# Optimization experiments

Measured on AMD Instinct MI355X. Metric: run time of the kernel, lower is better.

The kernel has to match this reference:

```python
import jax, jax.numpy as jnp
import numpy as np

N_NODES = 100000
N_EDGES = 3200000
D_IN = 128
D_HID = 128
N_CLASSES = 64
EPS = 0.0  # GINConv default


def setup_inputs() -> dict:
    key = jax.random.key(0)
    k1, k2, k3, k4, k5, k6 = jax.random.split(key, 6)
    x = jax.random.normal(k1, (N_NODES, D_IN), dtype=jnp.float32)
    edge_index = jax.random.randint(k2, (2, N_EDGES), 0, N_NODES, dtype=jnp.int64)
    s1 = 1.0 / np.sqrt(D_IN)
    W1 = jax.random.uniform(k3, (D_HID, D_IN), minval=-s1, maxval=s1, dtype=jnp.float32)
    b1 = jax.random.uniform(k4, (D_HID,), minval=-s1, maxval=s1, dtype=jnp.float32)
    s2 = 1.0 / np.sqrt(D_HID)
    W2 = jax.random.uniform(k5, (N_CLASSES, D_HID), minval=-s2, maxval=s2, dtype=jnp.float32)
    b2 = jax.random.uniform(k6, (N_CLASSES,), minval=-s2, maxval=s2, dtype=jnp.float32)
    return {"x": x, "edge_index": edge_index, "W1": W1, "b1": b1, "W2": W2, "b2": b2}


def gin_conv(h, src, dst, W, b):
    # sum_{j in N(i)} h_j  : scatter-add of source features into target nodes
    msgs = jnp.take(h, src, axis=0)                       # [E, D]
    agg = jax.ops.segment_sum(msgs, dst, num_segments=N_NODES)  # [N, D]
    z = (1.0 + EPS) * h + agg
    return z @ W.T + b


def reference(x, edge_index, W1, b1, W2, b2):
    src = edge_index[0]
    dst = edge_index[1]
    h = gin_conv(x, src, dst, W1, b1)
    h = jax.nn.relu(h)
    # dropout p=0.5 is identity in eval mode
    out = gin_conv(h, src, dst, W2, b2)
    return out
```

## Files before the change

kernel.cpp:

```cpp
#include <hip/hip_runtime.h>
#include <stdint.h>

#define NN 100000
#define NE 3200000
#define NBK 782
#define NB  512
#define CH  6250
#define CSRCAP 4800

typedef unsigned int uint;
typedef unsigned short ushort;
typedef __attribute__((ext_vector_type(8))) short bf16x8;
typedef __attribute__((ext_vector_type(4))) float f32x4;

static __device__ __forceinline__ float bflo(uint v) {
    uint u = v << 16; return __builtin_bit_cast(float, u);
}
static __device__ __forceinline__ float bfhi(uint v) {
    uint u = v & 0xffff0000u; return __builtin_bit_cast(float, u);
}
static __device__ __forceinline__ float bfraw(uint v) {
    return __builtin_bit_cast(float, v);
}
static __device__ __forceinline__ float b2f(ushort v) {
    uint u = ((uint)v) << 16; return __builtin_bit_cast(float, u);
}
static __device__ __forceinline__ ushort f2b(float f) {
    uint u = __builtin_bit_cast(uint, f);
    u += 0x7fffu + ((u >> 16) & 1u);
    return (ushort)(u >> 16);
}
static __device__ __forceinline__ int wscan(int v, int lane) {
#pragma unroll
    for (int off = 1; off < 64; off <<= 1) {
        int t = __shfl_up(v, off);
        if (lane >= off) v += t;
    }
    return v;
}


__global__ __launch_bounds__(512) void hist2_k(const int* __restrict__ ei,
                                               int* __restrict__ hist) {
    __shared__ int hl[NBK];
    int tid = threadIdx.x, b = blockIdx.x;
    for (int k = tid; k < NBK; k += 512) hl[k] = 0;
    __syncthreads();
    int base = b * CH;
    for (int i = base + tid; i < base + CH; i += 512)
        atomicAdd(&hl[ei[NE + i] >> 7], 1);
    __syncthreads();
    for (int k = tid; k < NBK; k += 512) hist[b * NBK + k] = hl[k];
}

__global__ __launch_bounds__(64) void pbase_k(const int* __restrict__ hist,
                                              int* __restrict__ pbase,
                                              int* __restrict__ totals) {
    int k = blockIdx.x, lane = threadIdx.x;
    int carry = 0;
#pragma unroll
    for (int c = 0; c < NB / 64; ++c) {
        int b = c * 64 + lane;
        int v = hist[b * NBK + k];
        int incl = wscan(v, lane);
        pbase[b * NBK + k] = carry + incl - v;
        carry += __shfl(incl, 63);
    }
    if (lane == 0) totals[k] = carry;
}

__global__ __launch_bounds__(1024) void bscan_k(const int* __restrict__ totals,
                                                int* __restrict__ gbase,
                                                int* __restrict__ nodeptr,
                                                ushort* __restrict__ y1,
                                                ushort* __restrict__ y2) {
    __shared__ int sd[1024];
    int t = threadIdx.x;
    int v = (t < NBK) ? totals[t] : 0;
    sd[t] = v;
    __syncthreads();
    for (int off = 1; off < 1024; off <<= 1) {
        int u = (t >= off) ? sd[t - off] : 0;
        __syncthreads();
        sd[t] += u;
        __syncthreads();
    }
    int excl = sd[t] - v;
    if (t < NBK) gbase[t] = excl;
    if (t == 0) { gbase[NBK] = NE; nodeptr[NN] = NE; }
    if (t < 64) ((uint*)(y1 + (size_t)NN * 128))[t] = 0;
    if (t < 32) ((uint*)(y2 + (size_t)NN * 64))[t] = 0;
}

__global__ __launch_bounds__(512) void bfill2_k(const int* __restrict__ ei,
                                                const int* __restrict__ pbase,
                                                const int* __restrict__ gbase,
                                                uint* __restrict__ barr) {
    __shared__ int cur[NBK];
    int tid = threadIdx.x, b = blockIdx.x;
    for (int k = tid; k < NBK; k += 512)
        cur[k] = gbase[k] + pbase[b * NBK + k];
    __syncthreads();
    int base = b * CH;
    for (int i = base + tid; i < base + CH; i += 512) {
        int s = ei[i], d = ei[NE + i];
        int pos = atomicAdd(&cur[d >> 7], 1);
        barr[pos] = ((uint)(d & 127) << 17) | (uint)s;
    }
}

__global__ __launch_bounds__(256) void csr_k(const uint* __restrict__ barr,
                                             const int* __restrict__ gbase,
                                             int* __restrict__ nodeptr,
                                             uint* __restrict__ col) {
    __shared__ uint stg[CSRCAP];
    __shared__ int cnt[128], cur[128];
    int tid = threadIdx.x;
    int blk = blockIdx.x;
    int s0 = gbase[blk], s1 = gbase[blk + 1];
    int n = s1 - s0;
    bool fits = (n <= CSRCAP);
    if (tid < 128) cnt[tid] = 0;
    __syncthreads();
    if (fits) {
        for (int i = tid; i < n; i += 256) {
            uint e = barr[s0 + i];
            stg[i] = e;
            atomicAdd(&cnt[e >> 17], 1);
        }
    } else {
        for (int i = s0 + tid; i < s1; i += 256)
            atomicAdd(&cnt[barr[i] >> 17], 1);
    }
    __syncthreads();
    if (tid < 64) {
        int c0 = cnt[2 * tid], c1 = cnt[2 * tid + 1];
        int s = c0 + c1;
        int incl = wscan(s, tid);
        int excl = incl - s;
        cur[2 * tid] = excl;
        cur[2 * tid + 1] = excl + c0;
        int node = blk * 128 + 2 * tid;
        if (node < NN)     nodeptr[node]     = s0 + excl;
        if (node + 1 < NN) nodeptr[node + 1] = s0 + excl + c0;
    }
    __syncthreads();
    if (fits) {
        for (int i = tid; i < n; i += 256) {
            uint e = stg[i];
            int pos = s0 + atomicAdd(&cur[e >> 17], 1);
            col[pos] = e & 0x1FFFF;
        }
    } else {
        for (int i = s0 + tid; i < s1; i += 256) {
            uint e = barr[i];
            int pos = s0 + atomicAdd(&cur[e >> 17], 1);
            col[pos] = e & 0x1FFFF;
        }
    }
}

__global__ __launch_bounds__(256) void gemm1_k(const float* __restrict__ x,
                                               const float* __restrict__ W1,
                                               ushort* __restrict__ y1) {
    __shared__ ushort wl[128 * 136];
    int tid = threadIdx.x;
    for (int i = tid; i < 128 * 128; i += 256)
        wl[(i >> 7) * 136 + (i & 127)] = f2b(W1[i]);
    __syncthreads();

    int wave = tid >> 6, lane = tid & 63;
    int lr = lane & 15, lk = (lane >> 4) * 8;
    long rowbase = (long)blockIdx.x * 128 + wave * 32;

    f32x4 acc[2][8] = {};
    for (int kc = 0; kc < 128; kc += 32) {
        bf16x8 a[2];
#pragma unroll
        for (int m = 0; m < 2; m++) {
            long row = rowbase + m * 16 + lr;
            if (row > NN - 1) row = NN - 1;
            const float* p = x + row * 128 + kc + lk;
            float f[8];
            *(float4*)(f)     = *(const float4*)(p);
            *(float4*)(f + 4) = *(const float4*)(p + 4);
            bf16x8 t;
#pragma unroll
            for (int j = 0; j < 8; j++) t[j] = (short)f2b(f[j]);
            a[m] = t;
        }
#pragma unroll
        for (int nb = 0; nb < 8; nb++) {
            bf16x8 b = *(const bf16x8*)&wl[(nb * 16 + lr) * 136 + kc + lk];
            acc[0][nb] = __builtin_amdgcn_mfma_f32_16x16x32_bf16(a[0], b, acc[0][nb], 0, 0, 0);
            acc[1][nb] = __builtin_amdgcn_mfma_f32_16x16x32_bf16(a[1], b, acc[1][nb], 0, 0, 0);
        }
    }
    int rq = (lane >> 4) * 4;
#pragma unroll
    for (int m = 0; m < 2; m++) {
#pragma unroll
        for (int r = 0; r < 4; r++) {
            long row = rowbase + m * 16 + rq + r;
            if (row < NN) {
#pragma unroll
                for (int nb = 0; nb < 8; nb++)
                    y1[row * 128 + nb * 16 + lr] = f2b(acc[m][nb][r]);
            }
        }
    }
}

__global__ __launch_bounds__(256) void gemm2_k(const ushort* __restrict__ h,
                                               const float* __restrict__ W2,
                                               ushort* __restrict__ y2) {
    __shared__ ushort wl[64 * 136];
    int tid = threadIdx.x;
    for (int i = tid; i < 64 * 128; i += 256)
        wl[(i >> 7) * 136 + (i & 127)] = f2b(W2[i]);
    __syncthreads();

    int wave = tid >> 6, lane = tid & 63;
    int lr = lane & 15, lk = (lane >> 4) * 8;
    long rowbase = (long)blockIdx.x * 128 + wave * 32;

    f32x4 acc[2][4] = {};
    for (int kc = 0; kc < 128; kc += 32) {
        bf16x8 a[2];
#pragma unroll
        for (int m = 0; m < 2; m++) {
            long row = rowbase + m * 16 + lr;
            if (row > NN - 1) row = NN - 1;
            a[m] = *(const bf16x8*)(h + row * 128 + kc + lk);
        }
#pragma unroll
        for (int nb = 0; nb < 4; nb++) {
            bf16x8 b = *(const bf16x8*)&wl[(nb * 16 + lr) * 136 + kc + lk];
            acc[0][nb] = __builtin_amdgcn_mfma_f32_16x16x32_bf16(a[0], b, acc[0][nb], 0, 0, 0);
            acc[1][nb] = __builtin_amdgcn_mfma_f32_16x16x32_bf16(a[1], b, acc[1][nb], 0, 0, 0);
        }
    }
    int rq = (lane >> 4) * 4;
#pragma unroll
    for (int m = 0; m < 2; m++) {
#pragma unroll
        for (int r = 0; r < 4; r++) {
            long row = rowbase + m * 16 + rq + r;
            if (row < NN) {
#pragma unroll
                for (int nb = 0; nb < 4; nb++)
                    y2[row * 64 + nb * 16 + lr] = f2b(acc[m][nb][r]);
            }
        }
    }
}


__global__ __launch_bounds__(256) void agg1_k(const ushort* __restrict__ y1,
                                              const int* __restrict__ nodeptr,
                                              const uint* __restrict__ col,
                                              const float* __restrict__ b1,
                                              ushort* __restrict__ h) {
    int wid = (blockIdx.x * 256 + threadIdx.x) >> 6;
    int lane = threadIdx.x & 63;
    if (wid >= NN) return;
    int s0 = nodeptr[wid], s1 = nodeptr[wid + 1];
    int q = lane >> 4, r = lane & 15;

    float aLo[4] = {}, aHi[4] = {};
    const ushort* yr = y1 + r * 8;

    for (int i = s0; i < s1; i += 64) {
        int m = s1 - i; if (m > 64) m = 64;
        int sv = (lane < m) ? (int)col[i + lane] : NN;
        int jg = (m + 15) >> 4;
        for (int g = 0; g < jg; ++g) {
            int e0 = 16 * g + q;
            int sj0 = __shfl(sv, e0);
            int sj1 = __shfl(sv, e0 + 4);
            int sj2 = __shfl(sv, e0 + 8);
            int sj3 = __shfl(sv, e0 + 12);
            uint4 u0 = *(const uint4*)(yr + (size_t)sj0 * 128);
            uint4 u1 = *(const uint4*)(yr + (size_t)sj1 * 128);
            uint4 u2 = *(const uint4*)(yr + (size_t)sj2 * 128);
            uint4 u3 = *(const uint4*)(yr + (size_t)sj3 * 128);
            aLo[0] += bflo(u0.x); aHi[0] += bfraw(u0.x);
            aLo[1] += bflo(u0.y); aHi[1] += bfraw(u0.y);
            aLo[2] += bflo(u0.z); aHi[2] += bfraw(u0.z);
            aLo[3] += bflo(u0.w); aHi[3] += bfraw(u0.w);
            aLo[0] += bflo(u1.x); aHi[0] += bfraw(u1.x);
            aLo[1] += bflo(u1.y); aHi[1] += bfraw(u1.y);
            aLo[2] += bflo(u1.z); aHi[2] += bfraw(u1.z);
            aLo[3] += bflo(u1.w); aHi[3] += bfraw(u1.w);
            aLo[0] += bflo(u2.x); aHi[0] += bfraw(u2.x);
            aLo[1] += bflo(u2.y); aHi[1] += bfraw(u2.y);
            aLo[2] += bflo(u2.z); aHi[2] += bfraw(u2.z);
            aLo[3] += bflo(u2.w); aHi[3] += bfraw(u2.w);
            aLo[0] += bflo(u3.x); aHi[0] += bfraw(u3.x);
            aLo[1] += bflo(u3.y); aHi[1] += bfraw(u3.y);
            aLo[2] += bflo(u3.z); aHi[2] += bfraw(u3.z);
            aLo[3] += bflo(u3.w); aHi[3] += bfraw(u3.w);
        }
    }
#pragma unroll
    for (int d = 0; d < 4; ++d) {
        aLo[d] += __shfl_xor(aLo[d], 16); aLo[d] += __shfl_xor(aLo[d], 32);
        aHi[d] += __shfl_xor(aHi[d], 16); aHi[d] += __shfl_xor(aHi[d], 32);
    }
    if (q == 0) {
        uint4 s = *(const uint4*)(y1 + (size_t)wid * 128 + r * 8);
        float4 bA = *(const float4*)(b1 + r * 8);
        float4 bB = *(const float4*)(b1 + r * 8 + 4);
        float v0 = fmaxf(aLo[0] + bflo(s.x) + bA.x, 0.f);
        float v1 = fmaxf(aHi[0] + bfhi(s.x) + bA.y, 0.f);
        float v2 = fmaxf(aLo[1] + bflo(s.y) + bA.z, 0.f);
        float v3 = fmaxf(aHi[1] + bfhi(s.y) + bA.w, 0.f);
        float v4 = fmaxf(aLo[2] + bflo(s.z) + bB.x, 0.f);
        float v5 = fmaxf(aHi[2] + bfhi(s.z) + bB.y, 0.f);
        float v6 = fmaxf(aLo[3] + bflo(s.w) + bB.z, 0.f);
        float v7 = fmaxf(aHi[3] + bfhi(s.w) + bB.w, 0.f);
        uint4 o;
        o.x = (uint)f2b(v0) | ((uint)f2b(v1) << 16);
        o.y = (uint)f2b(v2) | ((uint)f2b(v3) << 16);
        o.z = (uint)f2b(v4) | ((uint)f2b(v5) << 16);
        o.w = (uint)f2b(v6) | ((uint)f2b(v7) << 16);
        *(uint4*)(h + (size_t)wid * 128 + r * 8) = o;
    }
}

__global__ __launch_bounds__(256) void agg2_k(const ushort* __restrict__ y2,
                                              const int* __restrict__ nodeptr,
                                              const uint* __restrict__ col,
                                              const float* __restrict__ b2,
                                              float* __restrict__ out) {
    int wid = (blockIdx.x * 256 + threadIdx.x) >> 6;
    int lane = threadIdx.x & 63;
    if (wid >= NN) return;
    int s0 = nodeptr[wid], s1 = nodeptr[wid + 1];
    int q = lane >> 4, r = lane & 15;

    float aLo[2] = {}, aHi[2] = {};
    const ushort* yr = y2 + r * 4;

    for (int i = s0; i < s1; i += 64) {
        int m = s1 - i; if (m > 64) m = 64;
        int sv = (lane < m) ? (int)col[i + lane] : NN;
        int jg = (m + 15) >> 4;
        for (int g = 0; g < jg; ++g) {
            int e0 = 16 * g + q;
            int sj0 = __shfl(sv, e0);
            int sj1 = __shfl(sv, e0 + 4);
            int sj2 = __shfl(sv, e0 + 8);
            int sj3 = __shfl(sv, e0 + 12);
            uint2 u0 = *(const uint2*)(yr + (size_t)sj0 * 64);
            uint2 u1 = *(const uint2*)(yr + (size_t)sj1 * 64);
            uint2 u2 = *(const uint2*)(yr + (size_t)sj2 * 64);
            uint2 u3 = *(const uint2*)(yr + (size_t)sj3 * 64);
            aLo[0] += bflo(u0.x); aHi[0] += bfraw(u0.x);
            aLo[1] += bflo(u0.y); aHi[1] += bfraw(u0.y);
            aLo[0] += bflo(u1.x); aHi[0] += bfraw(u1.x);
            aLo[1] += bflo(u1.y); aHi[1] += bfraw(u1.y);
            aLo[0] += bflo(u2.x); aHi[0] += bfraw(u2.x);
            aLo[1] += bflo(u2.y); aHi[1] += bfraw(u2.y);
            aLo[0] += bflo(u3.x); aHi[0] += bfraw(u3.x);
            aLo[1] += bflo(u3.y); aHi[1] += bfraw(u3.y);
        }
    }
#pragma unroll
    for (int d = 0; d < 2; ++d) {
        aLo[d] += __shfl_xor(aLo[d], 16); aLo[d] += __shfl_xor(aLo[d], 32);
        aHi[d] += __shfl_xor(aHi[d], 16); aHi[d] += __shfl_xor(aHi[d], 32);
    }
    if (q == 0) {
        uint2 s = *(const uint2*)(y2 + (size_t)wid * 64 + r * 4);
        float4 bb = *(const float4*)(b2 + r * 4);
        float4 o;
        o.x = aLo[0] + bflo(s.x) + bb.x;
        o.y = aHi[0] + bfhi(s.x) + bb.y;
        o.z = aLo[1] + bflo(s.y) + bb.z;
        o.w = aHi[1] + bfhi(s.y) + bb.w;
        *(float4*)(out + (size_t)wid * 64 + r * 4) = o;
    }
}


static constexpr size_t alup(size_t x) { return (x + 255) & ~(size_t)255; }
static constexpr size_t OFF_HIST  = 0;
static constexpr size_t OFF_PBASE = alup(OFF_HIST  + (size_t)NB * NBK * 4);
static constexpr size_t OFF_TOT   = alup(OFF_PBASE + (size_t)NB * NBK * 4);
static constexpr size_t OFF_GBASE = alup(OFF_TOT   + NBK * 4);
static constexpr size_t OFF_NPTR  = alup(OFF_GBASE + (NBK + 1) * 4);
static constexpr size_t OFF_BARR  = alup(OFF_NPTR  + (size_t)(NN + 1) * 4);
static constexpr size_t OFF_COL   = alup(OFF_BARR  + (size_t)NE * 4);
static constexpr size_t OFF_Y1    = alup(OFF_COL   + (size_t)NE * 4);
static constexpr size_t OFF_H     = alup(OFF_Y1 + (size_t)(NN + 1) * 128 * 2);
static constexpr size_t OFF_Y2    = alup(OFF_H  + (size_t)NN * 128 * 2);

extern "C" void kernel_launch(void* const* d_in, const int* in_sizes, int n_in,
                              void* d_out, int out_size, void* d_ws, size_t ws_size,
                              hipStream_t stream) {
    const float* x  = (const float*)d_in[0];
    const int*   ei = (const int*)d_in[1];
    const float* W1 = (const float*)d_in[2];
    const float* b1 = (const float*)d_in[3];
    const float* W2 = (const float*)d_in[4];
    const float* b2 = (const float*)d_in[5];
    float* out = (float*)d_out;
    char* ws = (char*)d_ws;

    int*  hist  = (int*)(ws + OFF_HIST);
    int*  pbase = (int*)(ws + OFF_PBASE);
    int*  tot   = (int*)(ws + OFF_TOT);
    int*  gbase = (int*)(ws + OFF_GBASE);
    int*  nptr  = (int*)(ws + OFF_NPTR);
    uint* barr  = (uint*)(ws + OFF_BARR);
    uint* colA  = (uint*)(ws + OFF_COL);
    ushort* y1 = (ushort*)(ws + OFF_Y1);
    ushort* hh = (ushort*)(ws + OFF_H);
    ushort* y2 = (ushort*)(ws + OFF_Y2);

    hipLaunchKernelGGL(hist2_k,  dim3(NB),  dim3(512),  0, stream, ei, hist);
    hipLaunchKernelGGL(pbase_k,  dim3(NBK), dim3(64),   0, stream, hist, pbase, tot);
    hipLaunchKernelGGL(bscan_k,  dim3(1),   dim3(1024), 0, stream, tot, gbase, nptr, y1, y2);
    hipLaunchKernelGGL(bfill2_k, dim3(NB),  dim3(512),  0, stream, ei, pbase, gbase, barr);
    hipLaunchKernelGGL(csr_k,    dim3(NBK), dim3(256),  0, stream, barr, gbase, nptr, colA);

    hipLaunchKernelGGL(gemm1_k, dim3(782),  dim3(256), 0, stream, x, W1, y1);
    hipLaunchKernelGGL(agg1_k,  dim3(25000),dim3(256), 0, stream, y1, nptr, colA, b1, hh);
    hipLaunchKernelGGL(gemm2_k, dim3(782),  dim3(256), 0, stream, hh, W2, y2);
    hipLaunchKernelGGL(agg2_k,  dim3(25000),dim3(256), 0, stream, y2, nptr, colA, b2, out);
}
```

Before: 263.9 us.

## Split layer-1 features into two 64-wide halves to shrink gather working set

Stores the first layer's transformed features as two separate 64-column bf16 arrays, and runs the layer-1 aggregation twice, once per half. This keeps each gather pass's table (about 12.8 MB) small enough to stay resident in cache instead of a 25.6 MB table. Layer-2 aggregation is reworked so 8 lanes each load 16 bytes per row, with 8 edges per wave step. The cost is reading the CSR column indices twice and an extra kernel launch.

```diff
diff --git a/kernel.cpp b/kernel.cpp
--- a/kernel.cpp
+++ b/kernel.cpp
@@ -22,9 +22,6 @@
 static __device__ __forceinline__ float bfraw(uint v) {
     return __builtin_bit_cast(float, v);
 }
-static __device__ __forceinline__ float b2f(ushort v) {
-    uint u = ((uint)v) << 16; return __builtin_bit_cast(float, u);
-}
 static __device__ __forceinline__ ushort f2b(float f) {
     uint u = __builtin_bit_cast(uint, f);
     u += 0x7fffu + ((u >> 16) & 1u);
@@ -72,7 +69,8 @@
 __global__ __launch_bounds__(1024) void bscan_k(const int* __restrict__ totals,
                                                 int* __restrict__ gbase,
                                                 int* __restrict__ nodeptr,
-                                                ushort* __restrict__ y1,
+                                                ushort* __restrict__ y1a,
+                                                ushort* __restrict__ y1b,
                                                 ushort* __restrict__ y2) {
     __shared__ int sd[1024];
     int t = threadIdx.x;
@@ -88,8 +86,9 @@
     int excl = sd[t] - v;
     if (t < NBK) gbase[t] = excl;
     if (t == 0) { gbase[NBK] = NE; nodeptr[NN] = NE; }
-    if (t < 64) ((uint*)(y1 + (size_t)NN * 128))[t] = 0;
-    if (t < 32) ((uint*)(y2 + (size_t)NN * 64))[t] = 0;
+    if (t < 32)              ((uint*)(y1a + (size_t)NN * 64))[t] = 0;
+    else if (t < 64)         ((uint*)(y1b + (size_t)NN * 64))[t - 32] = 0;
+    else if (t < 96)         ((uint*)(y2  + (size_t)NN * 64))[t - 64] = 0;
 }
 
 __global__ __launch_bounds__(512) void bfill2_k(const int* __restrict__ ei,
@@ -162,7 +161,8 @@
 
 __global__ __launch_bounds__(256) void gemm1_k(const float* __restrict__ x,
                                                const float* __restrict__ W1,
-                                               ushort* __restrict__ y1) {
+                                               ushort* __restrict__ y1a,
+                                               ushort* __restrict__ y1b) {
     __shared__ ushort wl[128 * 136];
     int tid = threadIdx.x;
     for (int i = tid; i < 128 * 128; i += 256)
@@ -204,14 +204,18 @@
             long row = rowbase + m * 16 + rq + r;
             if (row < NN) {
 #pragma unroll
-                for (int nb = 0; nb < 8; nb++)
-                    y1[row * 128 + nb * 16 + lr] = f2b(acc[m][nb][r]);
+                for (int nb = 0; nb < 8; nb++) {
+                    ushort v = f2b(acc[m][nb][r]);
+                    if (nb < 4) y1a[row * 64 + nb * 16 + lr] = v;
+                    else        y1b[row * 64 + (nb - 4) * 16 + lr] = v;
+                }
             }
         }
     }
 }
 
-__global__ __launch_bounds__(256) void gemm2_k(const ushort* __restrict__ h,
+__global__ __launch_bounds__(256) void gemm2_k(const ushort* __restrict__ ha,
+                                               const ushort* __restrict__ hb,
                                                const float* __restrict__ W2,
                                                ushort* __restrict__ y2) {
     __shared__ ushort wl[64 * 136];
@@ -225,13 +229,16 @@
     long rowbase = (long)blockIdx.x * 128 + wave * 32;
 
     f32x4 acc[2][4] = {};
+#pragma unroll
     for (int kc = 0; kc < 128; kc += 32) {
+        const ushort* hsrc = (kc < 64) ? ha : hb;
+        int koff = kc & 63;
         bf16x8 a[2];
 #pragma unroll
         for (int m = 0; m < 2; m++) {
             long row = rowbase + m * 16 + lr;
             if (row > NN - 1) row = NN - 1;
-            a[m] = *(const bf16x8*)(h + row * 128 + kc + lk);
+            a[m] = *(const bf16x8*)(hsrc + row * 64 + koff + lk);
         }
 #pragma unroll
         for (int nb = 0; nb < 4; nb++) {
@@ -256,34 +263,34 @@
 }
 
 
-__global__ __launch_bounds__(256) void agg1_k(const ushort* __restrict__ y1,
-                                              const int* __restrict__ nodeptr,
-                                              const uint* __restrict__ col,
-                                              const float* __restrict__ b1,
-                                              ushort* __restrict__ h) {
+__global__ __launch_bounds__(256) void agg1h_k(const ushort* __restrict__ yh,
+                                               const int* __restrict__ nodeptr,
+                                               const uint* __restrict__ col,
+                                               const float* __restrict__ bh,
+                                               ushort* __restrict__ hh) {
     int wid = (blockIdx.x * 256 + threadIdx.x) >> 6;
     int lane = threadIdx.x & 63;
     if (wid >= NN) return;
     int s0 = nodeptr[wid], s1 = nodeptr[wid + 1];
-    int q = lane >> 4, r = lane & 15;
+    int o = lane >> 3, r = lane & 7;
 
     float aLo[4] = {}, aHi[4] = {};
-    const ushort* yr = y1 + r * 8;
+    const ushort* yr = yh + r * 8;
 
     for (int i = s0; i < s1; i += 64) {
         int m = s1 - i; if (m > 64) m = 64;
         int sv = (lane < m) ? (int)col[i + lane] : NN;
-        int jg = (m + 15) >> 4;
+        int jg = (m + 31) >> 5;
         for (int g = 0; g < jg; ++g) {
-            int e0 = 16 * g + q;
+            int e0 = 32 * g + o;
             int sj0 = __shfl(sv, e0);
-            int sj1 = __shfl(sv, e0 + 4);
-            int sj2 = __shfl(sv, e0 + 8);
-            int sj3 = __shfl(sv, e0 + 12);
-            uint4 u0 = *(const uint4*)(yr + (size_t)sj0 * 128);
-            uint4 u1 = *(const uint4*)(yr + (size_t)sj1 * 128);
-            uint4 u2 = *(const uint4*)(yr + (size_t)sj2 * 128);
-            uint4 u3 = *(const uint4*)(yr + (size_t)sj3 * 128);
+            int sj1 = __shfl(sv, e0 + 8);
+            int sj2 = __shfl(sv, e0 + 16);
+            int sj3 = __shfl(sv, e0 + 24);
+            uint4 u0 = *(const uint4*)(yr + (size_t)sj0 * 64);
+            uint4 u1 = *(const uint4*)(yr + (size_t)sj1 * 64);
+            uint4 u2 = *(const uint4*)(yr + (size_t)sj2 * 64);
+            uint4 u3 = *(const uint4*)(yr + (size_t)sj3 * 64);
             aLo[0] += bflo(u0.x); aHi[0] += bfraw(u0.x);
             aLo[1] += bflo(u0.y); aHi[1] += bfraw(u0.y);
             aLo[2] += bflo(u0.z); aHi[2] += bfraw(u0.z);
@@ -304,13 +311,14 @@
     }
 #pragma unroll
     for (int d = 0; d < 4; ++d) {
-        aLo[d] += __shfl_xor(aLo[d], 16); aLo[d] += __shfl_xor(aLo[d], 32);
-        aHi[d] += __shfl_xor(aHi[d], 16); aHi[d] += __shfl_xor(aHi[d], 32);
-    }
-    if (q == 0) {
-        uint4 s = *(const uint4*)(y1 + (size_t)wid * 128 + r * 8);
-        float4 bA = *(const float4*)(b1 + r * 8);
-        float4 bB = *(const float4*)(b1 + r * 8 + 4);
+        aLo[d] += __shfl_xor(aLo[d], 8);  aHi[d] += __shfl_xor(aHi[d], 8);
+        aLo[d] += __shfl_xor(aLo[d], 16); aHi[d] += __shfl_xor(aHi[d], 16);
+        aLo[d] += __shfl_xor(aLo[d], 32); aHi[d] += __shfl_xor(aHi[d], 32);
+    }
+    if (o == 0) {
+        uint4 s = *(const uint4*)(yh + (size_t)wid * 64 + r * 8);
+        float4 bA = *(const float4*)(bh + r * 8);
+        float4 bB = *(const float4*)(bh + r * 8 + 4);
         float v0 = fmaxf(aLo[0] + bflo(s.x) + bA.x, 0.f);
         float v1 = fmaxf(aHi[0] + bfhi(s.x) + bA.y, 0.f);
         float v2 = fmaxf(aLo[1] + bflo(s.y) + bA.z, 0.f);
@@ -319,12 +327,12 @@
         float v5 = fmaxf(aHi[2] + bfhi(s.z) + bB.y, 0.f);
         float v6 = fmaxf(aLo[3] + bflo(s.w) + bB.z, 0.f);
         float v7 = fmaxf(aHi[3] + bfhi(s.w) + bB.w, 0.f);
-        uint4 o;
-        o.x = (uint)f2b(v0) | ((uint)f2b(v1) << 16);
-        o.y = (uint)f2b(v2) | ((uint)f2b(v3) << 16);
-        o.z = (uint)f2b(v4) | ((uint)f2b(v5) << 16);
-        o.w = (uint)f2b(v6) | ((uint)f2b(v7) << 16);
-        *(uint4*)(h + (size_t)wid * 128 + r * 8) = o;
+        uint4 out;
+        out.x = (uint)f2b(v0) | ((uint)f2b(v1) << 16);
+        out.y = (uint)f2b(v2) | ((uint)f2b(v3) << 16);
+        out.z = (uint)f2b(v4) | ((uint)f2b(v5) << 16);
+        out.w = (uint)f2b(v6) | ((uint)f2b(v7) << 16);
+        *(uint4*)(hh + (size_t)wid * 64 + r * 8) = out;
     }
 }
 
@@ -337,49 +345,64 @@
     int lane = threadIdx.x & 63;
     if (wid >= NN) return;
     int s0 = nodeptr[wid], s1 = nodeptr[wid + 1];
-    int q = lane >> 4, r = lane & 15;
-
-    float aLo[2] = {}, aHi[2] = {};
-    const ushort* yr = y2 + r * 4;
+    int o = lane >> 3, r = lane & 7;
+
+    float aLo[4] = {}, aHi[4] = {};
+    const ushort* yr = y2 + r * 8;
 
     for (int i = s0; i < s1; i += 64) {
         int m = s1 - i; if (m > 64) m = 64;
         int sv = (lane < m) ? (int)col[i + lane] : NN;
-        int jg = (m + 15) >> 4;
+        int jg = (m + 31) >> 5;
         for (int g = 0; g < jg; ++g) {
-            int e0 = 16 * g + q;
+            int e0 = 32 * g + o;
             int sj0 = __shfl(sv, e0);
-            int sj1 = __shfl(sv, e0 + 4);
-            int sj2 = __shfl(sv, e0 + 8);
-            int sj3 = __shfl(sv, e0 + 12);
-            uint2 u0 = *(const uint2*)(yr + (size_t)sj0 * 64);
-            uint2 u1 = *(const uint2*)(yr + (size_t)sj1 * 64);
-            uint2 u2 = *(const uint2*)(yr + (size_t)sj2 * 64);
-            uint2 u3 = *(const uint2*)(yr + (size_t)sj3 * 64);
+            int sj1 = __shfl(sv, e0 + 8);
+            int sj2 = __shfl(sv, e0 + 16);
+            int sj3 = __shfl(sv, e0 + 24);
+            uint4 u0 = *(const uint4*)(yr + (size_t)sj0 * 64);
+            uint4 u1 = *(const uint4*)(yr + (size_t)sj1 * 64);
+            uint4 u2 = *(const uint4*)(yr + (size_t)sj2 * 64);
+            uint4 u3 = *(const uint4*)(yr + (size_t)sj3 * 64);
             aLo[0] += bflo(u0.x); aHi[0] += bfraw(u0.x);
             aLo[1] += bflo(u0.y); aHi[1] += bfraw(u0.y);
+            aLo[2] += bflo(u0.z); aHi[2] += bfraw(u0.z);
+            aLo[3] += bflo(u0.w); aHi[3] += bfraw(u0.w);
             aLo[0] += bflo(u1.x); aHi[0] += bfraw(u1.x);
             aLo[1] += bflo(u1.y); aHi[1] += bfraw(u1.y);
+            aLo[2] += bflo(u1.z); aHi[2] += bfraw(u1.z);
+            aLo[3] += bflo(u1.w); aHi[3] += bfraw(u1.w);
             aLo[0] += bflo(u2.x); aHi[0] += bfraw(u2.x);
             aLo[1] += bflo(u2.y); aHi[1] += bfraw(u2.y);
+            aLo[2] += bflo(u2.z); aHi[2] += bfraw(u2.z);
+            aLo[3] += bflo(u2.w); aHi[3] += bfraw(u2.w);
             aLo[0] += bflo(u3.x); aHi[0] += bfraw(u3.x);
             aLo[1] += bflo(u3.y); aHi[1] += bfraw(u3.y);
-        }
-    }
-#pragma unroll
-    for (int d = 0; d < 2; ++d) {
-        aLo[d] += __shfl_xor(aLo[d], 16); aLo[d] += __shfl_xor(aLo[d], 32);
-        aHi[d] += __shfl_xor(aHi[d], 16); aHi[d] += __shfl_xor(aHi[d], 32);
-    }
-    if (q == 0) {
-        uint2 s = *(const uint2*)(y2 + (size_t)wid * 64 + r * 4);
-        float4 bb = *(const float4*)(b2 + r * 4);
-        float4 o;
-        o.x = aLo[0] + bflo(s.x) + bb.x;
-        o.y = aHi[0] + bfhi(s.x) + bb.y;
-        o.z = aLo[1] + bflo(s.y) + bb.z;
-        o.w = aHi[1] + bfhi(s.y) + bb.w;
-        *(float4*)(out + (size_t)wid * 64 + r * 4) = o;
+            aLo[2] += bflo(u3.z); aHi[2] += bfraw(u3.z);
+            aLo[3] += bflo(u3.w); aHi[3] += bfraw(u3.w);
+        }
+    }
+#pragma unroll
+    for (int d = 0; d < 4; ++d) {
+        aLo[d] += __shfl_xor(aLo[d], 8);  aHi[d] += __shfl_xor(aHi[d], 8);
+        aLo[d] += __shfl_xor(aLo[d], 16); aHi[d] += __shfl_xor(aHi[d], 16);
+        aLo[d] += __shfl_xor(aLo[d], 32); aHi[d] += __shfl_xor(aHi[d], 32);
+    }
+    if (o == 0) {
+        uint4 s = *(const uint4*)(y2 + (size_t)wid * 64 + r * 8);
+        float4 bA = *(const float4*)(b2 + r * 8);
+        float4 bB = *(const float4*)(b2 + r * 8 + 4);
+        float4 o0, o1;
+        o0.x = aLo[0] + bflo(s.x) + bA.x;
+        o0.y = aHi[0] + bfhi(s.x) + bA.y;
+        o0.z = aLo[1] + bflo(s.y) + bA.z;
+        o0.w = aHi[1] + bfhi(s.y) + bA.w;
+        o1.x = aLo[2] + bflo(s.z) + bB.x;
+        o1.y = aHi[2] + bfhi(s.z) + bB.y;
+        o1.z = aLo[3] + bflo(s.w) + bB.z;
+        o1.w = aHi[3] + bfhi(s.w) + bB.w;
+        *(float4*)(out + (size_t)wid * 64 + r * 8)     = o0;
+        *(float4*)(out + (size_t)wid * 64 + r * 8 + 4) = o1;
     }
 }
 
@@ -392,9 +415,11 @@
 static constexpr size_t OFF_NPTR  = alup(OFF_GBASE + (NBK + 1) * 4);
 static constexpr size_t OFF_BARR  = alup(OFF_NPTR  + (size_t)(NN + 1) * 4);
 static constexpr size_t OFF_COL   = alup(OFF_BARR  + (size_t)NE * 4);
-static constexpr size_t OFF_Y1    = alup(OFF_COL   + (size_t)NE * 4);
-static constexpr size_t OFF_H     = alup(OFF_Y1 + (size_t)(NN + 1) * 128 * 2);
-static constexpr size_t OFF_Y2    = alup(OFF_H  + (size_t)NN * 128 * 2);
+static constexpr size_t OFF_Y1A   = alup(OFF_COL   + (size_t)NE * 4);
+static constexpr size_t OFF_Y1B   = alup(OFF_Y1A + (size_t)(NN + 1) * 64 * 2);
+static constexpr size_t OFF_HA    = alup(OFF_Y1B + (size_t)(NN + 1) * 64 * 2);
+static constexpr size_t OFF_HB    = alup(OFF_HA  + (size_t)(NN + 1) * 64 * 2);
+static constexpr size_t OFF_Y2    = alup(OFF_HB  + (size_t)(NN + 1) * 64 * 2);
 
 extern "C" void kernel_launch(void* const* d_in, const int* in_sizes, int n_in,
                               void* d_out, int out_size, void* d_ws, size_t ws_size,
@@ -415,18 +440,21 @@
     int*  nptr  = (int*)(ws + OFF_NPTR);
     uint* barr  = (uint*)(ws + OFF_BARR);
     uint* colA  = (uint*)(ws + OFF_COL);
-    ushort* y1 = (ushort*)(ws + OFF_Y1);
-    ushort* hh = (ushort*)(ws + OFF_H);
-    ushort* y2 = (ushort*)(ws + OFF_Y2);
+    ushort* y1a = (ushort*)(ws + OFF_Y1A);
+    ushort* y1b = (ushort*)(ws + OFF_Y1B);
+    ushort* ha  = (ushort*)(ws + OFF_HA);
+    ushort* hb  = (ushort*)(ws + OFF_HB);
+    ushort* y2  = (ushort*)(ws + OFF_Y2);
 
     hipLaunchKernelGGL(hist2_k,  dim3(NB),  dim3(512),  0, stream, ei, hist);
     hipLaunchKernelGGL(pbase_k,  dim3(NBK), dim3(64),   0, stream, hist, pbase, tot);
-    hipLaunchKernelGGL(bscan_k,  dim3(1),   dim3(1024), 0, stream, tot, gbase, nptr, y1, y2);
+    hipLaunchKernelGGL(bscan_k,  dim3(1),   dim3(1024), 0, stream, tot, gbase, nptr, y1a, y1b, y2);
     hipLaunchKernelGGL(bfill2_k, dim3(NB),  dim3(512),  0, stream, ei, pbase, gbase, barr);
     hipLaunchKernelGGL(csr_k,    dim3(NBK), dim3(256),  0, stream, barr, gbase, nptr, colA);
 
-    hipLaunchKernelGGL(gemm1_k, dim3(782),  dim3(256), 0, stream, x, W1, y1);
-    hipLaunchKernelGGL(agg1_k,  dim3(25000),dim3(256), 0, stream, y1, nptr, colA, b1, hh);
-    hipLaunchKernelGGL(gemm2_k, dim3(782),  dim3(256), 0, stream, hh, W2, y2);
+    hipLaunchKernelGGL(gemm1_k, dim3(782),  dim3(256), 0, stream, x, W1, y1a, y1b);
+    hipLaunchKernelGGL(agg1h_k, dim3(25000),dim3(256), 0, stream, y1a, nptr, colA, b1,      ha);
+    hipLaunchKernelGGL(agg1h_k, dim3(25000),dim3(256), 0, stream, y1b, nptr, colA, b1 + 64, hb);
+    hipLaunchKernelGGL(gemm2_k, dim3(782),  dim3(256), 0, stream, ha, hb, W2, y2);
     hipLaunchKernelGGL(agg2_k,  dim3(25000),dim3(256), 0, stream, y2, nptr, colA, b2, out);
 }
```

After: 258.4 us. 2.1% less time.
